# Kernel optimization log

Hardware: AMD Instinct MI355X
Metric: run time of the kernel (lower is better)

## Reference

```python
import jax, jax.numpy as jnp
import numpy as np

NUM_EMB = 1024
EMB_DIM = 256
COMM_COST = 0.25
BETA = 0.25


def setup_inputs() -> dict:
    key = jax.random.key(0)
    k1, k2 = jax.random.split(key)
    x = jax.random.normal(k1, (16, EMB_DIM, 64, 64), dtype=jnp.float32)
    # nn.Embedding initialized uniform(-1/num_emb, 1/num_emb)
    emb_weight = jax.random.uniform(
        k2, (NUM_EMB, EMB_DIM), dtype=jnp.float32,
        minval=-1.0 / NUM_EMB, maxval=1.0 / NUM_EMB)
    return {"x": x, "emb_weight": emb_weight}


def reference(x, emb_weight):
    # x: [B, C, H, W] -> [B, H, W, C]
    xp = jnp.transpose(x, (0, 2, 3, 1))
    B, H, W, C = xp.shape
    flat = xp.reshape(-1, C)  # [N, C]
    # squared euclidean distances (argmin-equivalent to torch.cdist)
    d2 = (jnp.sum(flat * flat, axis=1, keepdims=True)
          - 2.0 * jnp.einsum('nc,kc->nk', flat, emb_weight)
          + jnp.sum(emb_weight * emb_weight, axis=1))  # [N, K]
    idx = jnp.argmin(d2, axis=1)  # [N]
    quantized = emb_weight[idx].reshape(B, H, W, C)
    e_latent_loss = jnp.mean((jax.lax.stop_gradient(quantized) - xp) ** 2) * BETA
    q_latent_loss = jnp.mean((quantized - jax.lax.stop_gradient(xp)) ** 2)
    c_loss = q_latent_loss + COMM_COST * e_latent_loss
    # straight-through estimator
    quant_st = xp + jax.lax.stop_gradient(quantized - xp)
    quant_out = jnp.transpose(quant_st, (0, 3, 1, 2))  # [B, C, H, W]
    return (c_loss, quant_out)
```

## Files before the change

### kernel.cpp

```cpp
#include <hip/hip_runtime.h>
#include <hip/hip_bf16.h>
#include <cstdint>
#include <cstddef>

#define EMB_K   1024
#define EMB_C   256
#define HWB     4096
#define NPIX    65536

typedef __bf16 bf16x8 __attribute__((ext_vector_type(8)));
typedef float  f32x4  __attribute__((ext_vector_type(4)));
typedef float  f32x4a __attribute__((ext_vector_type(4), aligned(4)));

__device__ __forceinline__ unsigned short bf16bits(float v) {
  __hip_bfloat16 h = __float2bfloat16(v);
  return __builtin_bit_cast(unsigned short, h);
}

__global__ void k_emb(const float* __restrict__ emb, unsigned short* __restrict__ emb_bf,
                      float* __restrict__ enorm, float* __restrict__ loss,
                      unsigned* __restrict__ ctr) {
  int k = blockIdx.x;
  int c = threadIdx.x;
  if (k == 0 && c == 0) { *loss = 0.f; *ctr = 0u; }
  float v = emb[(size_t)k * EMB_C + c];
  emb_bf[(size_t)k * EMB_C + c] = bf16bits(v);
  float s = v * v;
  for (int m = 32; m; m >>= 1) s += __shfl_down(s, m, 64);
  __shared__ float red[4];
  int lane = c & 63, w = c >> 6;
  if (lane == 0) red[w] = s;
  __syncthreads();
  if (c == 0) enorm[k] = red[0] + red[1] + red[2] + red[3];
}

__global__ __launch_bounds__(256) void
k_tr(const float* __restrict__ x, unsigned short* __restrict__ A,
     float* __restrict__ xn_g) {
  __shared__ unsigned char tile[64 * 512];
  __shared__ float xn_l[64];
  int t  = threadIdx.x;
  int n0 = blockIdx.x * 64;
  int b  = n0 >> 12, hw0 = n0 & 4095;
  int nl = t & 63, qq = t >> 6;
  if (t < 64) xn_l[t] = 0.f;
  __syncthreads();
  const float* xp = x + (size_t)b * (EMB_C * HWB) + hw0 + nl;
  float xn = 0.f;
#pragma unroll
  for (int o = 0; o < 8; ++o) {
    int cc = qq * 8 + o;
    float v[8];
#pragma unroll
    for (int j = 0; j < 8; ++j) {
      v[j] = xp[(size_t)(cc * 8 + j) * HWB];
      xn += v[j] * v[j];
    }
    union { unsigned u[4]; uint4 q; } pk;
#pragma unroll
    for (int m = 0; m < 4; ++m)
      pk.u[m] = (unsigned)bf16bits(v[2 * m]) | ((unsigned)bf16bits(v[2 * m + 1]) << 16);
    int pos = ((cc >> 3) << 3) | ((cc & 7) ^ (nl & 7));
    *(uint4*)(tile + nl * 512 + pos * 16) = pk.q;
  }
  atomicAdd(&xn_l[nl], xn);
  __syncthreads();
  if (t < 64) xn_g[n0 + t] = xn_l[t];
  uint4* Adst = (uint4*)A + (size_t)n0 * 32;
#pragma unroll
  for (int k = 0; k < 8; ++k) {
    int id = k * 256 + t;
    int n = id >> 5, slot = id & 31;
    int pos = ((slot >> 3) << 3) | ((slot & 7) ^ (n & 7));
    Adst[id] = *(const uint4*)(tile + n * 512 + pos * 16);
  }
}

__device__ __forceinline__ void stage64(const unsigned short* __restrict__ rows,
                                        unsigned char* buf, int t) {
#pragma unroll
  for (int j = 0; j < 4; ++j) {
    int d = j * 512 + t;
    int r = d >> 5;
    int slot = d & 31;
    int c16 = ((slot >> 3) << 3) | ((slot & 7) ^ (r & 7));
    const unsigned short* src = rows + (size_t)r * EMB_C + c16 * 8;
    __builtin_amdgcn_global_load_lds(
        (const __attribute__((address_space(1))) void*)src,
        (__attribute__((address_space(3))) void*)(buf + (unsigned)(j * 8192 + (t >> 6) * 1024)),
        16, 0, 0);
  }
}

#define K2_LDS 70688

__global__ __launch_bounds__(512, 2) void
k_gemm(const unsigned short* __restrict__ A, const unsigned short* __restrict__ embbf,
       const float* __restrict__ enorm, const float* __restrict__ xn_g,
       unsigned* __restrict__ keys_g, float* __restrict__ out,
       float* __restrict__ loss, unsigned* __restrict__ ctr) {
  extern __shared__ char smem[];
  unsigned char* R0 = (unsigned char*)smem;
  unsigned char* R1 = (unsigned char*)(smem + 32768);
  float*    cjl    = (float*)(smem + 65536);
  unsigned* keys_l = (unsigned*)(smem + 69632);
  float*    xn_l   = (float*)(smem + 70144);
  float*    red    = (float*)(smem + 70656);

  int n0 = blockIdx.x * 128;
  int t = threadIdx.x, w = t >> 6, lane = t & 63;
  int quad = lane >> 4, lr = lane & 15;
  int g  = w >> 2;
  int h2 = w & 3;

  stage64(A + (size_t)n0 * EMB_C, R0, t);
  stage64(A + (size_t)(n0 + 64) * EMB_C, R1, t);
  for (int i = t; i < 1024; i += 512) cjl[i] = 0.375f - 0.5f * enorm[i];
  if (t < 128) { keys_l[t] = 0u; xn_l[t] = xn_g[n0 + t]; }
  __syncthreads();

  bf16x8 af[4][8];
#pragma unroll
  for (int i = 0; i < 4; ++i) {
    int rA = g * 64 + i * 16 + lr;
#pragma unroll
    for (int s = 0; s < 8; ++s) {
      int cc = s * 4 + quad;
      int pos = ((cc >> 3) << 3) | ((cc & 7) ^ (rA & 7));
      af[i][s] = *(const bf16x8*)(R0 + rA * 512 + pos * 16);
    }
  }
  __syncthreads();

  stage64(embbf, R0, t);
  __syncthreads();

  unsigned best[4][4] = {};
  for (int kt = 0; kt < 16; ++kt) {
    unsigned char* srcB = (kt & 1) ? R1 : R0;
    unsigned char* dstB = (kt & 1) ? R0 : R1;
    if (kt < 15) stage64(embbf + (size_t)(kt + 1) * 64 * EMB_C, dstB, t);
    float cj; unsigned kp;
    { int k = kt * 64 + h2 * 16 + lr; cj = cjl[k]; kp = 1023u - (unsigned)k; }
    f32x4 acc[4] = {};
#pragma unroll
    for (int s = 0; s < 8; ++s) {
      int cc = s * 4 + quad;
      int rB = h2 * 16 + lr;
      int pos = ((cc >> 3) << 3) | ((cc & 7) ^ (rB & 7));
      bf16x8 bf = *(const bf16x8*)(srcB + rB * 512 + pos * 16);
#pragma unroll
      for (int i = 0; i < 4; ++i)
        acc[i] = __builtin_amdgcn_mfma_f32_16x16x32_bf16(af[i][s], bf, acc[i], 0, 0, 0);
    }
#pragma unroll
    for (int i = 0; i < 4; ++i)
#pragma unroll
      for (int r = 0; r < 4; ++r) {
        float f = acc[i][r] + cj;
        unsigned key = (__float_as_uint(f) & 0xFFFFFC00u) | kp;
        best[i][r] = best[i][r] > key ? best[i][r] : key;
      }
    __syncthreads();
  }

#pragma unroll
  for (int i = 0; i < 4; ++i)
#pragma unroll
    for (int r = 0; r < 4; ++r) {
      unsigned v = best[i][r];
#pragma unroll
      for (int m = 1; m < 16; m <<= 1) {
        unsigned o = (unsigned)__shfl_xor((int)v, m, 64);
        v = v > o ? v : o;
      }
      if (lr == 0) atomicMax(&keys_l[g * 64 + i * 16 + quad * 4 + r], v);
    }
  __syncthreads();

  if (t < 128) {
    unsigned key = keys_l[t];
    keys_g[n0 + t] = key;
    float fh = __uint_as_float(key & 0xFFFFFC00u);
    float lsum = xn_l[t] + 0.75f - 2.0f * fh;
    for (int m = 32; m; m >>= 1) lsum += __shfl_down(lsum, m, 64);
    if (lane == 0) red[w] = lsum;
  }
  __syncthreads();
  if (t == 0) {
    atomicAdd(loss, red[0] + red[1]);
    __threadfence();
    unsigned done = atomicAdd(ctr, 1u);
    if (done == gridDim.x - 1) {
      float total = atomicAdd(loss, 0.f);
      out[0] = 1.0625f * total / 16777216.0f;
    }
  }
}

__global__ __launch_bounds__(512) void
k_out(const float* __restrict__ emb, const unsigned* __restrict__ keys_g,
      float* __restrict__ out) {
  extern __shared__ float tile[];
  int t  = threadIdx.x;
  int n0 = blockIdx.x * 256;
  int b  = n0 >> 12, hw0 = n0 & 4095;
  int w  = t >> 6, lane = t & 63;
  int n  = t >> 1, ch = t & 1;
  int idx = 1023 - (int)(keys_g[n0 + n] & 1023u);
  const float* er = emb + (size_t)idx * EMB_C;
  float* ob = out + 1 + (size_t)b * (EMB_C * HWB) + hw0;
  for (int p = 0; p < 4; ++p) {
    int c0 = p * 64;
    if (p) __syncthreads();
#pragma unroll
    for (int jj = 0; jj < 8; ++jj) {
      f32x4 q = *(const f32x4*)(er + c0 + ch * 32 + jj * 4);
#pragma unroll
      for (int m = 0; m < 4; ++m)
        tile[(ch * 32 + jj * 4 + m) * 256 + n] = q[m];
    }
    __syncthreads();
#pragma unroll
    for (int cc = 0; cc < 8; ++cc) {
      int cl = w * 8 + cc;
      f32x4 q = *(const f32x4*)(tile + cl * 256 + lane * 4);
      *(f32x4a*)(ob + (size_t)(c0 + cl) * HWB + lane * 4) = q;
    }
  }
}

extern "C" void kernel_launch(void* const* d_in, const int* in_sizes, int n_in,
                              void* d_out, int out_size, void* d_ws, size_t ws_size,
                              hipStream_t stream) {
  const float* x   = (const float*)d_in[0];
  const float* emb = (const float*)d_in[1];
  float* out = (float*)d_out;
  char*  ws  = (char*)d_ws;

  unsigned short* emb_bf = (unsigned short*)ws;
  float*          enorm  = (float*)(ws + 524288);
  float*          loss   = (float*)(ws + 528384);
  unsigned*       ctr    = (unsigned*)(ws + 528388);
  float*          xn_g   = (float*)(ws + 532480);
  unsigned*       keys_g = (unsigned*)(ws + 794624);

  unsigned short* A = (unsigned short*)(out + 4);

  hipFuncSetAttribute((const void*)k_gemm,
                      hipFuncAttributeMaxDynamicSharedMemorySize, K2_LDS);
  hipFuncSetAttribute((const void*)k_out,
                      hipFuncAttributeMaxDynamicSharedMemorySize, 65536);

  k_emb <<<dim3(EMB_K),      dim3(EMB_C), 0,      stream>>>(emb, emb_bf, enorm, loss, ctr);
  k_tr  <<<dim3(NPIX / 64),  dim3(256),   0,      stream>>>(x, A, xn_g);
  k_gemm<<<dim3(NPIX / 128), dim3(512),   K2_LDS, stream>>>(A, emb_bf, enorm, xn_g,
                                                            keys_g, out, loss, ctr);
  k_out <<<dim3(NPIX / 256), dim3(512),   65536,  stream>>>(emb, keys_g, out);
}
```

Measured before the change: 187.1 us.

## Load GEMM operands directly from global memory instead of staging through LDS

Drops the double-buffered LDS staging of the A tile and codebook tiles in the distance GEMM. Each lane now reads its bf16 fragments straight from global memory (through cache), and the per-iteration barriers are removed. Launch bounds are raised to allow four blocks per CU, since the LDS footprint falls to only a few KB. The trade-off is more global/L2 traffic and no explicit prefetch of codebook tiles, which may expose load latency in the MFMA loop.

```diff
diff --git a/kernel.cpp b/kernel.cpp
--- a/kernel.cpp
+++ b/kernel.cpp
@@ -76,36 +76,15 @@
   }
 }
 
-__device__ __forceinline__ void stage64(const unsigned short* __restrict__ rows,
-                                        unsigned char* buf, int t) {
-#pragma unroll
-  for (int j = 0; j < 4; ++j) {
-    int d = j * 512 + t;
-    int r = d >> 5;
-    int slot = d & 31;
-    int c16 = ((slot >> 3) << 3) | ((slot & 7) ^ (r & 7));
-    const unsigned short* src = rows + (size_t)r * EMB_C + c16 * 8;
-    __builtin_amdgcn_global_load_lds(
-        (const __attribute__((address_space(1))) void*)src,
-        (__attribute__((address_space(3))) void*)(buf + (unsigned)(j * 8192 + (t >> 6) * 1024)),
-        16, 0, 0);
-  }
-}
-
-#define K2_LDS 70688
-
-__global__ __launch_bounds__(512, 2) void
+__global__ __launch_bounds__(512, 4) void
 k_gemm(const unsigned short* __restrict__ A, const unsigned short* __restrict__ embbf,
        const float* __restrict__ enorm, const float* __restrict__ xn_g,
        unsigned* __restrict__ keys_g, float* __restrict__ out,
        float* __restrict__ loss, unsigned* __restrict__ ctr) {
-  extern __shared__ char smem[];
-  unsigned char* R0 = (unsigned char*)smem;
-  unsigned char* R1 = (unsigned char*)(smem + 32768);
-  float*    cjl    = (float*)(smem + 65536);
-  unsigned* keys_l = (unsigned*)(smem + 69632);
-  float*    xn_l   = (float*)(smem + 70144);
-  float*    red    = (float*)(smem + 70656);
+  __shared__ float    cjl[1024];
+  __shared__ unsigned keys_l[128];
+  __shared__ float    xn_l[128];
+  __shared__ float    red[8];
 
   int n0 = blockIdx.x * 128;
   int t = threadIdx.x, w = t >> 6, lane = t & 63;
@@ -113,42 +92,31 @@
   int g  = w >> 2;
   int h2 = w & 3;
 
-  stage64(A + (size_t)n0 * EMB_C, R0, t);
-  stage64(A + (size_t)(n0 + 64) * EMB_C, R1, t);
   for (int i = t; i < 1024; i += 512) cjl[i] = 0.375f - 0.5f * enorm[i];
   if (t < 128) { keys_l[t] = 0u; xn_l[t] = xn_g[n0 + t]; }
-  __syncthreads();
 
   bf16x8 af[4][8];
 #pragma unroll
   for (int i = 0; i < 4; ++i) {
-    int rA = g * 64 + i * 16 + lr;
+    const unsigned short* ar =
+        A + (size_t)(n0 + g * 64 + i * 16 + lr) * EMB_C + quad * 8;
+#pragma unroll
+    for (int s = 0; s < 8; ++s)
+      af[i][s] = *(const bf16x8*)(ar + s * 32);
+  }
+  __syncthreads();
+
+  unsigned best[4][4] = {};
+  const unsigned short* bbase = embbf + (size_t)(h2 * 16 + lr) * EMB_C + quad * 8;
+  for (int kt = 0; kt < 16; ++kt) {
+    const unsigned short* br = bbase + (size_t)kt * 64 * EMB_C;
+    int k = kt * 64 + h2 * 16 + lr;
+    float cj = cjl[k];
+    unsigned kp = 1023u - (unsigned)k;
+    f32x4 acc[4] = {};
 #pragma unroll
     for (int s = 0; s < 8; ++s) {
-      int cc = s * 4 + quad;
-      int pos = ((cc >> 3) << 3) | ((cc & 7) ^ (rA & 7));
-      af[i][s] = *(const bf16x8*)(R0 + rA * 512 + pos * 16);
-    }
-  }
-  __syncthreads();
-
-  stage64(embbf, R0, t);
-  __syncthreads();
-
-  unsigned best[4][4] = {};
-  for (int kt = 0; kt < 16; ++kt) {
-    unsigned char* srcB = (kt & 1) ? R1 : R0;
-    unsigned char* dstB = (kt & 1) ? R0 : R1;
-    if (kt < 15) stage64(embbf + (size_t)(kt + 1) * 64 * EMB_C, dstB, t);
-    float cj; unsigned kp;
-    { int k = kt * 64 + h2 * 16 + lr; cj = cjl[k]; kp = 1023u - (unsigned)k; }
-    f32x4 acc[4] = {};
-#pragma unroll
-    for (int s = 0; s < 8; ++s) {
-      int cc = s * 4 + quad;
-      int rB = h2 * 16 + lr;
-      int pos = ((cc >> 3) << 3) | ((cc & 7) ^ (rB & 7));
-      bf16x8 bf = *(const bf16x8*)(srcB + rB * 512 + pos * 16);
+      bf16x8 bf = *(const bf16x8*)(br + s * 32);
 #pragma unroll
       for (int i = 0; i < 4; ++i)
         acc[i] = __builtin_amdgcn_mfma_f32_16x16x32_bf16(af[i][s], bf, acc[i], 0, 0, 0);
@@ -161,8 +129,8 @@
         unsigned key = (__float_as_uint(f) & 0xFFFFFC00u) | kp;
         best[i][r] = best[i][r] > key ? best[i][r] : key;
       }
-    __syncthreads();
-  }
+  }
+  __syncthreads();
 
 #pragma unroll
   for (int i = 0; i < 4; ++i)
@@ -247,14 +215,12 @@
 
   unsigned short* A = (unsigned short*)(out + 4);
 
-  hipFuncSetAttribute((const void*)k_gemm,
-                      hipFuncAttributeMaxDynamicSharedMemorySize, K2_LDS);
   hipFuncSetAttribute((const void*)k_out,
                       hipFuncAttributeMaxDynamicSharedMemorySize, 65536);
 
-  k_emb <<<dim3(EMB_K),      dim3(EMB_C), 0,      stream>>>(emb, emb_bf, enorm, loss, ctr);
-  k_tr  <<<dim3(NPIX / 64),  dim3(256),   0,      stream>>>(x, A, xn_g);
-  k_gemm<<<dim3(NPIX / 128), dim3(512),   K2_LDS, stream>>>(A, emb_bf, enorm, xn_g,
-                                                            keys_g, out, loss, ctr);
-  k_out <<<dim3(NPIX / 256), dim3(512),   65536,  stream>>>(emb, keys_g, out);
-}
+  k_emb <<<dim3(EMB_K),      dim3(EMB_C), 0,     stream>>>(emb, emb_bf, enorm, loss, ctr);
+  k_tr  <<<dim3(NPIX / 64),  dim3(256),   0,     stream>>>(x, A, xn_g);
+  k_gemm<<<dim3(NPIX / 128), dim3(512),   0,     stream>>>(A, emb_bf, enorm, xn_g,
+                                                           keys_g, out, loss, ctr);
+  k_out <<<dim3(NPIX / 256), dim3(512),   65536, stream>>>(emb, keys_g, out);
+}
```

New measurement: 322.3 us. 1.72x slower.

## Fuse transpose, distance GEMM and output gather into one kernel

Applied to the files above, without the earlier changes.

Merges the transpose/bf16 conversion, the argmin GEMM and the output scatter into a single kernel that handles 256 pixels per block. The A operand and keys no longer round-trip through global memory. The codebook staging becomes a 4-deep LDS ring with explicit vmcnt waits, and each wave now covers 32 codes per tile. The cost is 137KB of LDS per block, which limits occupancy to one block per CU, and only 256 blocks are launched.

```diff
diff --git a/kernel.cpp b/kernel.cpp
--- a/kernel.cpp
+++ b/kernel.cpp
@@ -34,48 +34,6 @@
   if (c == 0) enorm[k] = red[0] + red[1] + red[2] + red[3];
 }
 
-__global__ __launch_bounds__(256) void
-k_tr(const float* __restrict__ x, unsigned short* __restrict__ A,
-     float* __restrict__ xn_g) {
-  __shared__ unsigned char tile[64 * 512];
-  __shared__ float xn_l[64];
-  int t  = threadIdx.x;
-  int n0 = blockIdx.x * 64;
-  int b  = n0 >> 12, hw0 = n0 & 4095;
-  int nl = t & 63, qq = t >> 6;
-  if (t < 64) xn_l[t] = 0.f;
-  __syncthreads();
-  const float* xp = x + (size_t)b * (EMB_C * HWB) + hw0 + nl;
-  float xn = 0.f;
-#pragma unroll
-  for (int o = 0; o < 8; ++o) {
-    int cc = qq * 8 + o;
-    float v[8];
-#pragma unroll
-    for (int j = 0; j < 8; ++j) {
-      v[j] = xp[(size_t)(cc * 8 + j) * HWB];
-      xn += v[j] * v[j];
-    }
-    union { unsigned u[4]; uint4 q; } pk;
-#pragma unroll
-    for (int m = 0; m < 4; ++m)
-      pk.u[m] = (unsigned)bf16bits(v[2 * m]) | ((unsigned)bf16bits(v[2 * m + 1]) << 16);
-    int pos = ((cc >> 3) << 3) | ((cc & 7) ^ (nl & 7));
-    *(uint4*)(tile + nl * 512 + pos * 16) = pk.q;
-  }
-  atomicAdd(&xn_l[nl], xn);
-  __syncthreads();
-  if (t < 64) xn_g[n0 + t] = xn_l[t];
-  uint4* Adst = (uint4*)A + (size_t)n0 * 32;
-#pragma unroll
-  for (int k = 0; k < 8; ++k) {
-    int id = k * 256 + t;
-    int n = id >> 5, slot = id & 31;
-    int pos = ((slot >> 3) << 3) | ((slot & 7) ^ (n & 7));
-    Adst[id] = *(const uint4*)(tile + n * 512 + pos * 16);
-  }
-}
-
 __device__ __forceinline__ void stage64(const unsigned short* __restrict__ rows,
                                         unsigned char* buf, int t) {
 #pragma unroll
@@ -92,77 +50,113 @@
   }
 }
 
-#define K2_LDS 70688
-
-__global__ __launch_bounds__(512, 2) void
-k_gemm(const unsigned short* __restrict__ A, const unsigned short* __restrict__ embbf,
-       const float* __restrict__ enorm, const float* __restrict__ xn_g,
-       unsigned* __restrict__ keys_g, float* __restrict__ out,
-       float* __restrict__ loss, unsigned* __restrict__ ctr) {
+#define LDS_BYTES 137280
+
+__global__ __launch_bounds__(512, 1) void
+k_main(const float* __restrict__ x, const float* __restrict__ emb,
+       const unsigned short* __restrict__ embbf, const float* __restrict__ enorm,
+       float* __restrict__ out, float* __restrict__ loss, unsigned* __restrict__ ctr) {
   extern __shared__ char smem[];
-  unsigned char* R0 = (unsigned char*)smem;
-  unsigned char* R1 = (unsigned char*)(smem + 32768);
-  float*    cjl    = (float*)(smem + 65536);
-  unsigned* keys_l = (unsigned*)(smem + 69632);
-  float*    xn_l   = (float*)(smem + 70144);
-  float*    red    = (float*)(smem + 70656);
-
-  int n0 = blockIdx.x * 128;
+  float*    cjl    = (float*)(smem + 131072);
+  unsigned* keys_l = (unsigned*)(smem + 135168);
+  float*    xn_l   = (float*)(smem + 136192);
+  float*    red    = (float*)(smem + 137216);
+
+  int n0 = blockIdx.x * 256;
+  int b  = n0 >> 12, hw0 = n0 & 4095;
   int t = threadIdx.x, w = t >> 6, lane = t & 63;
   int quad = lane >> 4, lr = lane & 15;
-  int g  = w >> 2;
-  int h2 = w & 3;
-
-  stage64(A + (size_t)n0 * EMB_C, R0, t);
-  stage64(A + (size_t)(n0 + 64) * EMB_C, R1, t);
+  int g  = w >> 1;
+  int h2 = w & 1;
+
   for (int i = t; i < 1024; i += 512) cjl[i] = 0.375f - 0.5f * enorm[i];
-  if (t < 128) { keys_l[t] = 0u; xn_l[t] = xn_g[n0 + t]; }
+  if (t < 256) { keys_l[t] = 0u; xn_l[t] = 0.f; }
   __syncthreads();
 
   bf16x8 af[4][8];
 #pragma unroll
-  for (int i = 0; i < 4; ++i) {
-    int rA = g * 64 + i * 16 + lr;
+  for (int p = 0; p < 2; ++p) {
+    if (p) __syncthreads();
+    {
+      int nl = ((t >> 6) & 1) * 64 + lane;
+      const float* xp = x + (size_t)b * (EMB_C * HWB) + hw0 + p * 128 + nl;
+      float xn = 0.f;
+#pragma unroll
+      for (int o = 0; o < 8; ++o) {
+        int cc = (t >> 7) * 8 + o;
+        float v[8];
+#pragma unroll
+        for (int j = 0; j < 8; ++j) {
+          v[j] = xp[(size_t)(cc * 8 + j) * HWB];
+          xn += v[j] * v[j];
+        }
+        union { unsigned u[4]; uint4 q; } pk;
+#pragma unroll
+        for (int m = 0; m < 4; ++m)
+          pk.u[m] = (unsigned)bf16bits(v[2 * m]) | ((unsigned)bf16bits(v[2 * m + 1]) << 16);
+        int pos = ((cc >> 3) << 3) | ((cc & 7) ^ (nl & 7));
+        *(uint4*)(smem + nl * 512 + pos * 16) = pk.q;
+      }
+      atomicAdd(&xn_l[p * 128 + nl], xn);
+    }
+    __syncthreads();
+    if ((g >> 1) == p) {
+#pragma unroll
+      for (int i = 0; i < 4; ++i) {
+        int rA = (g & 1) * 64 + i * 16 + lr;
+#pragma unroll
+        for (int s = 0; s < 8; ++s) {
+          int cc = s * 4 + quad;
+          int pos = ((cc >> 3) << 3) | ((cc & 7) ^ (rA & 7));
+          af[i][s] = *(const bf16x8*)(smem + rA * 512 + pos * 16);
+        }
+      }
+    }
+  }
+  __syncthreads();
+
+  stage64(embbf,                (unsigned char*)smem,         t);
+  stage64(embbf + 64 * EMB_C,   (unsigned char*)smem + 32768, t);
+  unsigned best[4][4] = {};
+#pragma unroll
+  for (int kt = 0; kt < 16; ++kt) {
+    if (kt < 14)
+      stage64(embbf + (size_t)(kt + 2) * 64 * EMB_C,
+              (unsigned char*)smem + (((kt + 2) & 3) << 15), t);
+    if (kt < 14)       asm volatile("s_waitcnt vmcnt(8)" ::: "memory");
+    else if (kt == 14) asm volatile("s_waitcnt vmcnt(4)" ::: "memory");
+    else               asm volatile("s_waitcnt vmcnt(0)" ::: "memory");
+    __builtin_amdgcn_s_barrier();
+    const unsigned char* sb = (const unsigned char*)smem + ((kt & 3) << 15);
+    int k0 = kt * 64 + h2 * 32 + lr;
+    float cj0 = cjl[k0], cj1 = cjl[k0 + 16];
+    unsigned kp0 = 1023u - (unsigned)k0, kp1 = kp0 - 16u;
+    f32x4 a0[4] = {}, a1[4] = {};
 #pragma unroll
     for (int s = 0; s < 8; ++s) {
       int cc = s * 4 + quad;
-      int pos = ((cc >> 3) << 3) | ((cc & 7) ^ (rA & 7));
-      af[i][s] = *(const bf16x8*)(R0 + rA * 512 + pos * 16);
-    }
-  }
-  __syncthreads();
-
-  stage64(embbf, R0, t);
-  __syncthreads();
-
-  unsigned best[4][4] = {};
-  for (int kt = 0; kt < 16; ++kt) {
-    unsigned char* srcB = (kt & 1) ? R1 : R0;
-    unsigned char* dstB = (kt & 1) ? R0 : R1;
-    if (kt < 15) stage64(embbf + (size_t)(kt + 1) * 64 * EMB_C, dstB, t);
-    float cj; unsigned kp;
-    { int k = kt * 64 + h2 * 16 + lr; cj = cjl[k]; kp = 1023u - (unsigned)k; }
-    f32x4 acc[4] = {};
-#pragma unroll
-    for (int s = 0; s < 8; ++s) {
-      int cc = s * 4 + quad;
-      int rB = h2 * 16 + lr;
-      int pos = ((cc >> 3) << 3) | ((cc & 7) ^ (rB & 7));
-      bf16x8 bf = *(const bf16x8*)(srcB + rB * 512 + pos * 16);
-#pragma unroll
-      for (int i = 0; i < 4; ++i)
-        acc[i] = __builtin_amdgcn_mfma_f32_16x16x32_bf16(af[i][s], bf, acc[i], 0, 0, 0);
+      int pos = ((cc >> 3) << 3) | ((cc & 7) ^ (lr & 7));
+      bf16x8 b0 = *(const bf16x8*)(sb + (h2 * 32 + lr) * 512 + pos * 16);
+      bf16x8 b1 = *(const bf16x8*)(sb + (h2 * 32 + 16 + lr) * 512 + pos * 16);
+#pragma unroll
+      for (int i = 0; i < 4; ++i) {
+        a0[i] = __builtin_amdgcn_mfma_f32_16x16x32_bf16(af[i][s], b0, a0[i], 0, 0, 0);
+        a1[i] = __builtin_amdgcn_mfma_f32_16x16x32_bf16(af[i][s], b1, a1[i], 0, 0, 0);
+      }
     }
 #pragma unroll
     for (int i = 0; i < 4; ++i)
 #pragma unroll
       for (int r = 0; r < 4; ++r) {
-        float f = acc[i][r] + cj;
-        unsigned key = (__float_as_uint(f) & 0xFFFFFC00u) | kp;
-        best[i][r] = best[i][r] > key ? best[i][r] : key;
-      }
-    __syncthreads();
-  }
+        float f0 = a0[i][r] + cj0;
+        unsigned key0 = (__float_as_uint(f0) & 0xFFFFFC00u) | kp0;
+        best[i][r] = best[i][r] > key0 ? best[i][r] : key0;
+        float f1 = a1[i][r] + cj1;
+        unsigned key1 = (__float_as_uint(f1) & 0xFFFFFC00u) | kp1;
+        best[i][r] = best[i][r] > key1 ? best[i][r] : key1;
+      }
+  }
+  __syncthreads();
 
 #pragma unroll
   for (int i = 0; i < 4; ++i)
@@ -178,9 +172,8 @@
     }
   __syncthreads();
 
-  if (t < 128) {
+  if (t < 256) {
     unsigned key = keys_l[t];
-    keys_g[n0 + t] = key;
     float fh = __uint_as_float(key & 0xFFFFFC00u);
     float lsum = xn_l[t] + 0.75f - 2.0f * fh;
     for (int m = 32; m; m >>= 1) lsum += __shfl_down(lsum, m, 64);
@@ -188,26 +181,13 @@
   }
   __syncthreads();
   if (t == 0) {
-    atomicAdd(loss, red[0] + red[1]);
+    atomicAdd(loss, red[0] + red[1] + red[2] + red[3]);
     __threadfence();
-    unsigned done = atomicAdd(ctr, 1u);
-    if (done == gridDim.x - 1) {
-      float total = atomicAdd(loss, 0.f);
-      out[0] = 1.0625f * total / 16777216.0f;
-    }
-  }
-}
-
-__global__ __launch_bounds__(512) void
-k_out(const float* __restrict__ emb, const unsigned* __restrict__ keys_g,
-      float* __restrict__ out) {
-  extern __shared__ float tile[];
-  int t  = threadIdx.x;
-  int n0 = blockIdx.x * 256;
-  int b  = n0 >> 12, hw0 = n0 & 4095;
-  int w  = t >> 6, lane = t & 63;
+  }
+
+  float* tile = (float*)smem;
   int n  = t >> 1, ch = t & 1;
-  int idx = 1023 - (int)(keys_g[n0 + n] & 1023u);
+  int idx = 1023 - (int)(keys_l[n] & 1023u);
   const float* er = emb + (size_t)idx * EMB_C;
   float* ob = out + 1 + (size_t)b * (EMB_C * HWB) + hw0;
   for (int p = 0; p < 4; ++p) {
@@ -226,6 +206,14 @@
       int cl = w * 8 + cc;
       f32x4 q = *(const f32x4*)(tile + cl * 256 + lane * 4);
       *(f32x4a*)(ob + (size_t)(c0 + cl) * HWB + lane * 4) = q;
+    }
+  }
+
+  if (t == 0) {
+    unsigned done = atomicAdd(ctr, 1u);
+    if (done == gridDim.x - 1) {
+      float total = atomicAdd(loss, 0.f);
+      out[0] = 1.0625f * total / 16777216.0f;
     }
   }
 }
@@ -242,19 +230,11 @@
   float*          enorm  = (float*)(ws + 524288);
   float*          loss   = (float*)(ws + 528384);
   unsigned*       ctr    = (unsigned*)(ws + 528388);
-  float*          xn_g   = (float*)(ws + 532480);
-  unsigned*       keys_g = (unsigned*)(ws + 794624);
-
-  unsigned short* A = (unsigned short*)(out + 4);
-
-  hipFuncSetAttribute((const void*)k_gemm,
-                      hipFuncAttributeMaxDynamicSharedMemorySize, K2_LDS);
-  hipFuncSetAttribute((const void*)k_out,
-                      hipFuncAttributeMaxDynamicSharedMemorySize, 65536);
-
-  k_emb <<<dim3(EMB_K),      dim3(EMB_C), 0,      stream>>>(emb, emb_bf, enorm, loss, ctr);
-  k_tr  <<<dim3(NPIX / 64),  dim3(256),   0,      stream>>>(x, A, xn_g);
-  k_gemm<<<dim3(NPIX / 128), dim3(512),   K2_LDS, stream>>>(A, emb_bf, enorm, xn_g,
-                                                            keys_g, out, loss, ctr);
-  k_out <<<dim3(NPIX / 256), dim3(512),   65536,  stream>>>(emb, keys_g, out);
-}
+
+  hipFuncSetAttribute((const void*)k_main,
+                      hipFuncAttributeMaxDynamicSharedMemorySize, LDS_BYTES);
+
+  k_emb <<<dim3(EMB_K),      dim3(EMB_C), 0,         stream>>>(emb, emb_bf, enorm, loss, ctr);
+  k_main<<<dim3(NPIX / 256), dim3(512),   LDS_BYTES, stream>>>(x, emb, emb_bf, enorm,
+                                                               out, loss, ctr);
+}
```

Result: slower. 207.5 us (+10.9%).
